# Performance work log

Hardware: AMD Instinct MI355X
Metric: run time of the kernel (lower is better)

Reference implementation:

```python
import jax, jax.numpy as jnp
import numpy as np

N_NODES = 100000
N_EDGES = 1600000
HIDDEN = 128
OUT = 64
NUM_LAYERS = 3


def setup_inputs() -> dict:
    key = jax.random.key(0)
    k1, k2, k3 = jax.random.split(key, 3)
    x = jax.random.normal(k1, (N_NODES, HIDDEN), dtype=jnp.float32)
    edge_index = jax.random.randint(k2, (2, N_EDGES), 0, N_NODES, dtype=jnp.int64)
    W = jax.random.normal(k3, (OUT, HIDDEN), dtype=jnp.float32) * (1.0 / np.sqrt(HIDDEN))
    b = jnp.zeros((OUT,), dtype=jnp.float32)
    return {"x": x, "edge_index": edge_index, "W": W, "b": b}


def reference(x, edge_index, W, b):
    n = x.shape[0]
    row, col = edge_index[0], edge_index[1]
    # degree of destination nodes (bincount over row), clamped to >= 1
    deg = jax.ops.segment_sum(jnp.ones_like(row, dtype=x.dtype), row, num_segments=n)
    deg_inv_sqrt = jnp.clip(deg, 1.0, None) ** -0.5
    norm = (deg_inv_sqrt[row] * deg_inv_sqrt[col])[:, None]  # [E, 1]

    def propagate(h):
        # gather -> scale -> scatter-add
        return jax.ops.segment_sum(h[col] * norm, row, num_segments=n)

    embs = [x]
    h = x
    for _ in range(NUM_LAYERS):
        h = propagate(h)
        embs.append(h)
    out = jnp.mean(jnp.stack(embs, axis=0), axis=0)  # [N, HIDDEN]
    return out @ W.T + b
```

## Files before the change

kernel.cpp:

```cpp
#include <hip/hip_runtime.h>

#define N_NODES 100000
#define N_EDGES 1600000
#define HIDDEN  128
#define OUTF    64
#define SLOT    48

#define EDGE4BLKS ((N_EDGES / 4 + 255) / 256)
#define NODEBLKS  ((N_NODES + 255) / 256)

__device__ __forceinline__ unsigned short f2bf(float f) {
    unsigned u = __float_as_uint(f);
    u += 0x7fffu + ((u >> 16) & 1u);
    return (unsigned short)(u >> 16);
}
__device__ __forceinline__ float2 bfp2f(unsigned p) {
    return make_float2(__uint_as_float(p << 16), __uint_as_float(p & 0xffff0000u));
}

__global__ void prep_kernel(const float* __restrict__ W, float* __restrict__ Wt,
                            int4* __restrict__ cnt4,
                            int4* __restrict__ z0d, int4* __restrict__ z1d,
                            int4* __restrict__ z2d) {
    int bid = blockIdx.x, tid = threadIdx.x;
    if (bid < 98) {
        int i = bid * 256 + tid;
        if (i < N_NODES / 4) cnt4[i] = make_int4(0, 0, 0, 0);
    } else if (bid < 130) {
        int i = (bid - 98) * 256 + tid;
        if (i < HIDDEN * OUTF) {
            int o = i / HIDDEN, k = i % HIDDEN;
            Wt[k * OUTF + o] = W[i];
        }
    } else {
        if (tid < 8)       z0d[tid]      = make_int4(0, 0, 0, 0);
        else if (tid < 16) z1d[tid - 8]  = make_int4(0, 0, 0, 0);
        else if (tid < 24) z2d[tid - 16] = make_int4(0, 0, 0, 0);
    }
}

#define GR    64
#define BK    32
#define HSP   36
#define WTP   68
__global__ __launch_bounds__(256) void mega_a_kernel(const float* __restrict__ x,
                                                     const float* __restrict__ Wt,
                                                     unsigned short* __restrict__ y0,
                                                     const int* __restrict__ ei,
                                                     int* __restrict__ cnt,
                                                     int* __restrict__ rank) {
    __shared__ float hs[GR * HSP];
    __shared__ float wt[BK * WTP];
    int tid = threadIdx.x;

    if (blockIdx.x & 1) {
        int cb = blockIdx.x >> 1;
        int t  = cb * 256 + tid;
        int e0 = t * 4;
        if (e0 + 3 < N_EDGES) {
            int4 r4 = *(const int4*)(ei + e0);
            int k0 = atomicAdd(&cnt[r4.x], 1);
            int k1 = atomicAdd(&cnt[r4.y], 1);
            int k2 = atomicAdd(&cnt[r4.z], 1);
            int k3 = atomicAdd(&cnt[r4.w], 1);
            *(int4*)(rank + e0) = make_int4(k0, k1, k2, k3);
        } else {
            for (int e = e0; e < N_EDGES; ++e) rank[e] = atomicAdd(&cnt[ei[e]], 1);
        }
        return;
    }

    int rowBase = (blockIdx.x >> 1) * GR;
    int o4 = (tid & 15) * 4;
    int rq = (tid >> 4) * 4;
    float4 a0 = {0,0,0,0}, a1 = {0,0,0,0}, a2 = {0,0,0,0}, a3 = {0,0,0,0};

    for (int kt = 0; kt < HIDDEN / BK; ++kt) {
        if (kt) __syncthreads();
        int kbase = kt * BK;
        #pragma unroll
        for (int t = 0; t < 2; ++t) {
            int f = tid + t * 256;
            int r = f >> 3, c4 = (f & 7) * 4;
            int row = rowBase + r;
            float4 v = (row < N_NODES) ? *(const float4*)(x + (size_t)row * HIDDEN + kbase + c4)
                                       : make_float4(0.f, 0.f, 0.f, 0.f);
            *(float4*)&hs[r * HSP + c4] = v;
        }
        #pragma unroll
        for (int t = 0; t < 2; ++t) {
            int f = tid + t * 256;
            int k = f >> 4, c4 = (f & 15) * 4;
            float4 v = *(const float4*)(Wt + (size_t)(kbase + k) * OUTF + c4);
            *(float4*)&wt[k * WTP + c4] = v;
        }
        __syncthreads();
        #pragma unroll 8
        for (int kk = 0; kk < BK; ++kk) {
            float4 wv = *(const float4*)&wt[kk * WTP + o4];
            float h0 = hs[(rq + 0) * HSP + kk];
            float h1 = hs[(rq + 1) * HSP + kk];
            float h2 = hs[(rq + 2) * HSP + kk];
            float h3 = hs[(rq + 3) * HSP + kk];
            a0.x += h0 * wv.x; a0.y += h0 * wv.y; a0.z += h0 * wv.z; a0.w += h0 * wv.w;
            a1.x += h1 * wv.x; a1.y += h1 * wv.y; a1.z += h1 * wv.z; a1.w += h1 * wv.w;
            a2.x += h2 * wv.x; a2.y += h2 * wv.y; a2.z += h2 * wv.z; a2.w += h2 * wv.w;
            a3.x += h3 * wv.x; a3.y += h3 * wv.y; a3.z += h3 * wv.z; a3.w += h3 * wv.w;
        }
    }
    int row = rowBase + rq;
    #pragma unroll
    for (int r = 0; r < 4; ++r) {
        if (row + r < N_NODES) {
            float4 a = (r == 0) ? a0 : (r == 1) ? a1 : (r == 2) ? a2 : a3;
            ushort4 s = {f2bf(a.x), f2bf(a.y), f2bf(a.z), f2bf(a.w)};
            *(ushort4*)&y0[(size_t)(row + r) * OUTF + o4] = s;
        }
    }
}

__global__ void mega_b_kernel(const int* __restrict__ ei,
                              const int* __restrict__ rank,
                              int* __restrict__ csr,
                              const int* __restrict__ cnt,
                              float* __restrict__ dinv,
                              float* __restrict__ rdinv) {
    int bid = blockIdx.x, tid = threadIdx.x;
    if (bid < EDGE4BLKS) {
        int t  = bid * 256 + tid;
        int e0 = t * 4;
        if (e0 + 3 < N_EDGES) {
            int4 r4 = *(const int4*)(ei + e0);
            int4 c4 = *(const int4*)(ei + N_EDGES + e0);
            int4 k4 = *(const int4*)(rank + e0);
            if (k4.x < SLOT) csr[r4.x * SLOT + k4.x] = c4.x;
            if (k4.y < SLOT) csr[r4.y * SLOT + k4.y] = c4.y;
            if (k4.z < SLOT) csr[r4.z * SLOT + k4.z] = c4.z;
            if (k4.w < SLOT) csr[r4.w * SLOT + k4.w] = c4.w;
        } else {
            for (int e = e0; e < N_EDGES; ++e) {
                int k = rank[e];
                if (k < SLOT) csr[ei[e] * SLOT + k] = ei[N_EDGES + e];
            }
        }
    } else {
        int i = (bid - EDGE4BLKS) * 256 + tid;
        if (i < N_NODES) {
            int deg  = cnt[i];
            float d  = fmaxf((float)deg, 1.0f);
            dinv[i]  = rsqrtf(d);
            rdinv[i] = sqrtf(d);
            if (i == 0) dinv[N_NODES] = 0.0f;
            int dc = deg > SLOT ? SLOT : deg;
            int dp = (dc + 7) & ~7;
            #pragma unroll
            for (int j = 0; j < 7; ++j)
                if (dc + j < dp) csr[i * SLOT + dc + j] = N_NODES;
        }
    }
}

__global__ __launch_bounds__(256) void pull1_kernel(const int* __restrict__ cnt,
                                                    const int* __restrict__ csr,
                                                    const float* __restrict__ dinv,
                                                    const unsigned short* __restrict__ y0,
                                                    unsigned short* __restrict__ z1) {
    int node = blockIdx.x * 4 + (threadIdx.x >> 6);
    int lane = threadIdx.x & 63;
    if (node >= N_NODES) return;
    int half = lane >> 5;
    int fp   = (lane & 31) * 2;
    int deg  = cnt[node];
    if (deg > SLOT) deg = SLOT;
    int degp = (deg + 7) & ~7;
    int s = node * SLOT;
    int e = s + degp;
    float2 acc = make_float2(0.f, 0.f);
    int i = s;
    for (; i + 15 < e; i += 16) {
        int c0 = csr[i      + half];
        int c1 = csr[i +  2 + half];
        int c2 = csr[i +  4 + half];
        int c3 = csr[i +  6 + half];
        int c4 = csr[i +  8 + half];
        int c5 = csr[i + 10 + half];
        int c6 = csr[i + 12 + half];
        int c7 = csr[i + 14 + half];
        float d0 = dinv[c0], d1 = dinv[c1], d2 = dinv[c2], d3 = dinv[c3];
        float d4 = dinv[c4], d5 = dinv[c5], d6 = dinv[c6], d7 = dinv[c7];
        unsigned p0 = *(const unsigned*)(y0 + (size_t)c0 * OUTF + fp);
        unsigned p1 = *(const unsigned*)(y0 + (size_t)c1 * OUTF + fp);
        unsigned p2 = *(const unsigned*)(y0 + (size_t)c2 * OUTF + fp);
        unsigned p3 = *(const unsigned*)(y0 + (size_t)c3 * OUTF + fp);
        unsigned p4 = *(const unsigned*)(y0 + (size_t)c4 * OUTF + fp);
        unsigned p5 = *(const unsigned*)(y0 + (size_t)c5 * OUTF + fp);
        unsigned p6 = *(const unsigned*)(y0 + (size_t)c6 * OUTF + fp);
        unsigned p7 = *(const unsigned*)(y0 + (size_t)c7 * OUTF + fp);
        float2 v0 = bfp2f(p0), v1 = bfp2f(p1), v2 = bfp2f(p2), v3 = bfp2f(p3);
        float2 v4 = bfp2f(p4), v5 = bfp2f(p5), v6 = bfp2f(p6), v7 = bfp2f(p7);
        acc.x += d0*v0.x + d1*v1.x + d2*v2.x + d3*v3.x + d4*v4.x + d5*v5.x + d6*v6.x + d7*v7.x;
        acc.y += d0*v0.y + d1*v1.y + d2*v2.y + d3*v3.y + d4*v4.y + d5*v5.y + d6*v6.y + d7*v7.y;
    }
    if (i < e) {
        int c0 = csr[i     + half];
        int c1 = csr[i + 2 + half];
        int c2 = csr[i + 4 + half];
        int c3 = csr[i + 6 + half];
        float d0 = dinv[c0], d1 = dinv[c1], d2 = dinv[c2], d3 = dinv[c3];
        unsigned p0 = *(const unsigned*)(y0 + (size_t)c0 * OUTF + fp);
        unsigned p1 = *(const unsigned*)(y0 + (size_t)c1 * OUTF + fp);
        unsigned p2 = *(const unsigned*)(y0 + (size_t)c2 * OUTF + fp);
        unsigned p3 = *(const unsigned*)(y0 + (size_t)c3 * OUTF + fp);
        float2 v0 = bfp2f(p0), v1 = bfp2f(p1), v2 = bfp2f(p2), v3 = bfp2f(p3);
        acc.x += d0*v0.x + d1*v1.x + d2*v2.x + d3*v3.x;
        acc.y += d0*v0.y + d1*v1.y + d2*v2.y + d3*v3.y;
    }
    acc.x += __shfl_xor(acc.x, 32);
    acc.y += __shfl_xor(acc.y, 32);
    if (lane < 32) {
        float dn = dinv[node];
        float zs = dn * dn;
        ushort2 o = {f2bf(acc.x * zs), f2bf(acc.y * zs)};
        *(ushort2*)(z1 + (size_t)node * OUTF + fp) = o;
    }
}

__global__ __launch_bounds__(256) void pull_kernel(const int* __restrict__ cnt,
                                                   const int* __restrict__ csr,
                                                   const float* __restrict__ dinv,
                                                   const unsigned short* __restrict__ zsrc,
                                                   unsigned short* __restrict__ zdst) {
    int node = blockIdx.x * 4 + (threadIdx.x >> 6);
    int lane = threadIdx.x & 63;
    if (node >= N_NODES) return;
    int half = lane >> 5;
    int fp   = (lane & 31) * 2;
    int deg  = cnt[node];
    if (deg > SLOT) deg = SLOT;
    int degp = (deg + 7) & ~7;
    int s = node * SLOT;
    int e = s + degp;
    float2 acc = make_float2(0.f, 0.f);
    int i = s;
    for (; i + 15 < e; i += 16) {
        int c0 = csr[i      + half];
        int c1 = csr[i +  2 + half];
        int c2 = csr[i +  4 + half];
        int c3 = csr[i +  6 + half];
        int c4 = csr[i +  8 + half];
        int c5 = csr[i + 10 + half];
        int c6 = csr[i + 12 + half];
        int c7 = csr[i + 14 + half];
        unsigned p0 = *(const unsigned*)(zsrc + (size_t)c0 * OUTF + fp);
        unsigned p1 = *(const unsigned*)(zsrc + (size_t)c1 * OUTF + fp);
        unsigned p2 = *(const unsigned*)(zsrc + (size_t)c2 * OUTF + fp);
        unsigned p3 = *(const unsigned*)(zsrc + (size_t)c3 * OUTF + fp);
        unsigned p4 = *(const unsigned*)(zsrc + (size_t)c4 * OUTF + fp);
        unsigned p5 = *(const unsigned*)(zsrc + (size_t)c5 * OUTF + fp);
        unsigned p6 = *(const unsigned*)(zsrc + (size_t)c6 * OUTF + fp);
        unsigned p7 = *(const unsigned*)(zsrc + (size_t)c7 * OUTF + fp);
        float2 v0 = bfp2f(p0), v1 = bfp2f(p1), v2 = bfp2f(p2), v3 = bfp2f(p3);
        float2 v4 = bfp2f(p4), v5 = bfp2f(p5), v6 = bfp2f(p6), v7 = bfp2f(p7);
        acc.x += (v0.x + v1.x) + (v2.x + v3.x) + (v4.x + v5.x) + (v6.x + v7.x);
        acc.y += (v0.y + v1.y) + (v2.y + v3.y) + (v4.y + v5.y) + (v6.y + v7.y);
    }
    if (i < e) {
        int c0 = csr[i     + half];
        int c1 = csr[i + 2 + half];
        int c2 = csr[i + 4 + half];
        int c3 = csr[i + 6 + half];
        unsigned p0 = *(const unsigned*)(zsrc + (size_t)c0 * OUTF + fp);
        unsigned p1 = *(const unsigned*)(zsrc + (size_t)c1 * OUTF + fp);
        unsigned p2 = *(const unsigned*)(zsrc + (size_t)c2 * OUTF + fp);
        unsigned p3 = *(const unsigned*)(zsrc + (size_t)c3 * OUTF + fp);
        float2 v0 = bfp2f(p0), v1 = bfp2f(p1), v2 = bfp2f(p2), v3 = bfp2f(p3);
        acc.x += (v0.x + v1.x) + (v2.x + v3.x);
        acc.y += (v0.y + v1.y) + (v2.y + v3.y);
    }
    acc.x += __shfl_xor(acc.x, 32);
    acc.y += __shfl_xor(acc.y, 32);
    if (lane < 32) {
        float dn = dinv[node];
        float zs = dn * dn;
        ushort2 o = {f2bf(acc.x * zs), f2bf(acc.y * zs)};
        *(ushort2*)(zdst + (size_t)node * OUTF + fp) = o;
    }
}

__global__ __launch_bounds__(256) void pull_merge_kernel(const int* __restrict__ cnt,
                                                         const int* __restrict__ csr,
                                                         const float* __restrict__ dinv,
                                                         const float* __restrict__ rdinv,
                                                         const unsigned short* __restrict__ y0,
                                                         const unsigned short* __restrict__ z1,
                                                         const unsigned short* __restrict__ z2,
                                                         const float* __restrict__ b,
                                                         float* __restrict__ out) {
    int node = blockIdx.x * 4 + (threadIdx.x >> 6);
    int lane = threadIdx.x & 63;
    if (node >= N_NODES) return;
    int half = lane >> 5;
    int fp   = (lane & 31) * 2;
    int deg  = cnt[node];
    if (deg > SLOT) deg = SLOT;
    int degp = (deg + 7) & ~7;
    int s = node * SLOT;
    int e = s + degp;
    float2 acc = make_float2(0.f, 0.f);
    int i = s;
    for (; i + 15 < e; i += 16) {
        int c0 = csr[i      + half];
        int c1 = csr[i +  2 + half];
        int c2 = csr[i +  4 + half];
        int c3 = csr[i +  6 + half];
        int c4 = csr[i +  8 + half];
        int c5 = csr[i + 10 + half];
        int c6 = csr[i + 12 + half];
        int c7 = csr[i + 14 + half];
        unsigned p0 = *(const unsigned*)(z2 + (size_t)c0 * OUTF + fp);
        unsigned p1 = *(const unsigned*)(z2 + (size_t)c1 * OUTF + fp);
        unsigned p2 = *(const unsigned*)(z2 + (size_t)c2 * OUTF + fp);
        unsigned p3 = *(const unsigned*)(z2 + (size_t)c3 * OUTF + fp);
        unsigned p4 = *(const unsigned*)(z2 + (size_t)c4 * OUTF + fp);
        unsigned p5 = *(const unsigned*)(z2 + (size_t)c5 * OUTF + fp);
        unsigned p6 = *(const unsigned*)(z2 + (size_t)c6 * OUTF + fp);
        unsigned p7 = *(const unsigned*)(z2 + (size_t)c7 * OUTF + fp);
        float2 v0 = bfp2f(p0), v1 = bfp2f(p1), v2 = bfp2f(p2), v3 = bfp2f(p3);
        float2 v4 = bfp2f(p4), v5 = bfp2f(p5), v6 = bfp2f(p6), v7 = bfp2f(p7);
        acc.x += (v0.x + v1.x) + (v2.x + v3.x) + (v4.x + v5.x) + (v6.x + v7.x);
        acc.y += (v0.y + v1.y) + (v2.y + v3.y) + (v4.y + v5.y) + (v6.y + v7.y);
    }
    if (i < e) {
        int c0 = csr[i     + half];
        int c1 = csr[i + 2 + half];
        int c2 = csr[i + 4 + half];
        int c3 = csr[i + 6 + half];
        unsigned p0 = *(const unsigned*)(z2 + (size_t)c0 * OUTF + fp);
        unsigned p1 = *(const unsigned*)(z2 + (size_t)c1 * OUTF + fp);
        unsigned p2 = *(const unsigned*)(z2 + (size_t)c2 * OUTF + fp);
        unsigned p3 = *(const unsigned*)(z2 + (size_t)c3 * OUTF + fp);
        float2 v0 = bfp2f(p0), v1 = bfp2f(p1), v2 = bfp2f(p2), v3 = bfp2f(p3);
        acc.x += (v0.x + v1.x) + (v2.x + v3.x);
        acc.y += (v0.y + v1.y) + (v2.y + v3.y);
    }
    acc.x += __shfl_xor(acc.x, 32);
    acc.y += __shfl_xor(acc.y, 32);
    if (lane < 32) {
        size_t idx = (size_t)node * OUTF + fp;
        float rd = rdinv[node];
        float dn = dinv[node];
        float2 s0 = bfp2f(*(const unsigned*)(y0 + idx));
        float2 s1 = bfp2f(*(const unsigned*)(z1 + idx));
        float2 s2 = bfp2f(*(const unsigned*)(z2 + idx));
        float2 bv = *(const float2*)(b + fp);
        float2 r;
        r.x = 0.25f * ((dn * s0.x + s1.x + s2.x) * rd + dn * acc.x) + bv.x;
        r.y = 0.25f * ((dn * s0.y + s1.y + s2.y) * rd + dn * acc.y) + bv.y;
        *(float2*)(out + idx) = r;
    }
}

extern "C" void kernel_launch(void* const* d_in, const int* in_sizes, int n_in,
                              void* d_out, int out_size, void* d_ws, size_t ws_size,
                              hipStream_t stream) {
    const float* x  = (const float*)d_in[0];
    const int*   ei = (const int*)d_in[1];
    const float* W  = (const float*)d_in[2];
    const float* b  = (const float*)d_in[3];
    float*       out = (float*)d_out;

    const size_t ZROWS = (size_t)N_NODES + 1;
    unsigned short* y0 = (unsigned short*)d_ws;
    unsigned short* z1 = y0 + ZROWS * OUTF;
    unsigned short* z2 = z1 + ZROWS * OUTF;
    float* Wt      = (float*)(z2 + ZROWS * OUTF);
    int*   csr     = (int*)(Wt + HIDDEN * OUTF);
    int*   cnt     = csr + (size_t)N_NODES * SLOT;
    float* dinv    = (float*)(cnt + N_NODES);
    float* rdinv   = dinv + (N_NODES + 1);

    int* rank = (int*)z2;

    const int BLK = 256;
    const int pullBlocks = (N_NODES + 3) / 4;

    prep_kernel<<<131, BLK, 0, stream>>>(W, Wt, (int4*)cnt,
                                         (int4*)(y0 + (size_t)N_NODES * OUTF),
                                         (int4*)(z1 + (size_t)N_NODES * OUTF),
                                         (int4*)(z2 + (size_t)N_NODES * OUTF));
    mega_a_kernel<<<2 * EDGE4BLKS, BLK, 0, stream>>>(x, Wt, y0, ei, cnt, rank);
    mega_b_kernel<<<EDGE4BLKS + NODEBLKS, BLK, 0, stream>>>(ei, rank, csr, cnt, dinv, rdinv);
    pull1_kernel<<<pullBlocks, BLK, 0, stream>>>(cnt, csr, dinv, y0, z1);
    pull_kernel<<<pullBlocks, BLK, 0, stream>>>(cnt, csr, dinv, z1, z2);
    pull_merge_kernel<<<pullBlocks, BLK, 0, stream>>>(cnt, csr, dinv, rdinv,
                                                      y0, z1, z2, b, out);
}
```

Before: 297.1 us.

## Pack four nodes per wavefront with 16-byte vectorized bf16 row gathers

The pull kernels are rewritten so each 64-lane wavefront handles four nodes instead of one. Each node gets 16 lanes: 8 lanes of 16-byte feature chunks times 2 edge parities. Gathers of bf16 rows become uint4 loads with eight float accumulators per lane, and the first two pull kernels are merged into one template. This cuts the number of load instructions and raises memory-level parallelism for low-degree nodes. The cost is higher register pressure, and lanes within a wavefront may diverge when their nodes have different degrees.

```diff
diff --git a/kernel.cpp b/kernel.cpp
--- a/kernel.cpp
+++ b/kernel.cpp
@@ -8,6 +8,7 @@
 
 #define EDGE4BLKS ((N_EDGES / 4 + 255) / 256)
 #define NODEBLKS  ((N_NODES + 255) / 256)
+#define PULLBLKS  ((N_NODES + 15) / 16)
 
 __device__ __forceinline__ unsigned short f2bf(float f) {
     unsigned u = __float_as_uint(f);
@@ -16,6 +17,9 @@
 }
 __device__ __forceinline__ float2 bfp2f(unsigned p) {
     return make_float2(__uint_as_float(p << 16), __uint_as_float(p & 0xffff0000u));
+}
+__device__ __forceinline__ unsigned packbf(float a, float b) {
+    return (unsigned)f2bf(a) | ((unsigned)f2bf(b) << 16);
 }
 
 __global__ void prep_kernel(const float* __restrict__ W, float* __restrict__ Wt,
@@ -160,203 +164,172 @@
     }
 }
 
-__global__ __launch_bounds__(256) void pull1_kernel(const int* __restrict__ cnt,
-                                                    const int* __restrict__ csr,
-                                                    const float* __restrict__ dinv,
-                                                    const unsigned short* __restrict__ y0,
-                                                    unsigned short* __restrict__ z1) {
-    int node = blockIdx.x * 4 + (threadIdx.x >> 6);
+template<bool SC>
+__global__ __launch_bounds__(256) void pull_v2_kernel(const int* __restrict__ cnt,
+                                                      const int* __restrict__ csr,
+                                                      const float* __restrict__ dinv,
+                                                      const unsigned short* __restrict__ zsrc,
+                                                      unsigned short* __restrict__ zdst) {
     int lane = threadIdx.x & 63;
-    if (node >= N_NODES) return;
-    int half = lane >> 5;
-    int fp   = (lane & 31) * 2;
-    int deg  = cnt[node];
+    int wid  = (blockIdx.x * blockDim.x + threadIdx.x) >> 6;
+    int g    = lane >> 3;
+    int node = wid * 4 + (g >> 1);
+    int par  = g & 1;
+    int fo   = (lane & 7) * 8;
+    bool valid = node < N_NODES;
+    int deg = valid ? cnt[node] : 0;
     if (deg > SLOT) deg = SLOT;
     int degp = (deg + 7) & ~7;
     int s = node * SLOT;
-    int e = s + degp;
-    float2 acc = make_float2(0.f, 0.f);
-    int i = s;
-    for (; i + 15 < e; i += 16) {
-        int c0 = csr[i      + half];
-        int c1 = csr[i +  2 + half];
-        int c2 = csr[i +  4 + half];
-        int c3 = csr[i +  6 + half];
-        int c4 = csr[i +  8 + half];
-        int c5 = csr[i + 10 + half];
-        int c6 = csr[i + 12 + half];
-        int c7 = csr[i + 14 + half];
-        float d0 = dinv[c0], d1 = dinv[c1], d2 = dinv[c2], d3 = dinv[c3];
-        float d4 = dinv[c4], d5 = dinv[c5], d6 = dinv[c6], d7 = dinv[c7];
-        unsigned p0 = *(const unsigned*)(y0 + (size_t)c0 * OUTF + fp);
-        unsigned p1 = *(const unsigned*)(y0 + (size_t)c1 * OUTF + fp);
-        unsigned p2 = *(const unsigned*)(y0 + (size_t)c2 * OUTF + fp);
-        unsigned p3 = *(const unsigned*)(y0 + (size_t)c3 * OUTF + fp);
-        unsigned p4 = *(const unsigned*)(y0 + (size_t)c4 * OUTF + fp);
-        unsigned p5 = *(const unsigned*)(y0 + (size_t)c5 * OUTF + fp);
-        unsigned p6 = *(const unsigned*)(y0 + (size_t)c6 * OUTF + fp);
-        unsigned p7 = *(const unsigned*)(y0 + (size_t)c7 * OUTF + fp);
-        float2 v0 = bfp2f(p0), v1 = bfp2f(p1), v2 = bfp2f(p2), v3 = bfp2f(p3);
-        float2 v4 = bfp2f(p4), v5 = bfp2f(p5), v6 = bfp2f(p6), v7 = bfp2f(p7);
-        acc.x += d0*v0.x + d1*v1.x + d2*v2.x + d3*v3.x + d4*v4.x + d5*v5.x + d6*v6.x + d7*v7.x;
-        acc.y += d0*v0.y + d1*v1.y + d2*v2.y + d3*v3.y + d4*v4.y + d5*v5.y + d6*v6.y + d7*v7.y;
-    }
-    if (i < e) {
-        int c0 = csr[i     + half];
-        int c1 = csr[i + 2 + half];
-        int c2 = csr[i + 4 + half];
-        int c3 = csr[i + 6 + half];
-        float d0 = dinv[c0], d1 = dinv[c1], d2 = dinv[c2], d3 = dinv[c3];
-        unsigned p0 = *(const unsigned*)(y0 + (size_t)c0 * OUTF + fp);
-        unsigned p1 = *(const unsigned*)(y0 + (size_t)c1 * OUTF + fp);
-        unsigned p2 = *(const unsigned*)(y0 + (size_t)c2 * OUTF + fp);
-        unsigned p3 = *(const unsigned*)(y0 + (size_t)c3 * OUTF + fp);
-        float2 v0 = bfp2f(p0), v1 = bfp2f(p1), v2 = bfp2f(p2), v3 = bfp2f(p3);
-        acc.x += d0*v0.x + d1*v1.x + d2*v2.x + d3*v3.x;
-        acc.y += d0*v0.y + d1*v1.y + d2*v2.y + d3*v3.y;
-    }
-    acc.x += __shfl_xor(acc.x, 32);
-    acc.y += __shfl_xor(acc.y, 32);
-    if (lane < 32) {
+    float a0=0.f,a1=0.f,a2=0.f,a3=0.f,a4=0.f,a5=0.f,a6=0.f,a7=0.f;
+
+    int e16 = degp & ~15;
+    int i = 0;
+    for (; i < e16; i += 16) {
+        int c0 = csr[s + i +  0 + par];
+        int c1 = csr[s + i +  2 + par];
+        int c2 = csr[s + i +  4 + par];
+        int c3 = csr[s + i +  6 + par];
+        int c4 = csr[s + i +  8 + par];
+        int c5 = csr[s + i + 10 + par];
+        int c6 = csr[s + i + 12 + par];
+        int c7 = csr[s + i + 14 + par];
+        float d0=1.f,d1=1.f,d2=1.f,d3=1.f,d4=1.f,d5=1.f,d6=1.f,d7=1.f;
+        if (SC) {
+            d0 = dinv[c0]; d1 = dinv[c1]; d2 = dinv[c2]; d3 = dinv[c3];
+            d4 = dinv[c4]; d5 = dinv[c5]; d6 = dinv[c6]; d7 = dinv[c7];
+        }
+        uint4 p0 = *(const uint4*)(zsrc + (size_t)c0 * OUTF + fo);
+        uint4 p1 = *(const uint4*)(zsrc + (size_t)c1 * OUTF + fo);
+        uint4 p2 = *(const uint4*)(zsrc + (size_t)c2 * OUTF + fo);
+        uint4 p3 = *(const uint4*)(zsrc + (size_t)c3 * OUTF + fo);
+        uint4 p4 = *(const uint4*)(zsrc + (size_t)c4 * OUTF + fo);
+        uint4 p5 = *(const uint4*)(zsrc + (size_t)c5 * OUTF + fo);
+        uint4 p6 = *(const uint4*)(zsrc + (size_t)c6 * OUTF + fo);
+        uint4 p7 = *(const uint4*)(zsrc + (size_t)c7 * OUTF + fo);
+        #define ACC(P, D) { \
+            float2 q0 = bfp2f(P.x), q1 = bfp2f(P.y), q2 = bfp2f(P.z), q3 = bfp2f(P.w); \
+            a0 += D*q0.x; a1 += D*q0.y; a2 += D*q1.x; a3 += D*q1.y; \
+            a4 += D*q2.x; a5 += D*q2.y; a6 += D*q3.x; a7 += D*q3.y; }
+        ACC(p0, d0) ACC(p1, d1) ACC(p2, d2) ACC(p3, d3)
+        ACC(p4, d4) ACC(p5, d5) ACC(p6, d6) ACC(p7, d7)
+    }
+    if (degp & 8) {
+        int c0 = csr[s + i + 0 + par];
+        int c1 = csr[s + i + 2 + par];
+        int c2 = csr[s + i + 4 + par];
+        int c3 = csr[s + i + 6 + par];
+        float d0=1.f,d1=1.f,d2=1.f,d3=1.f;
+        if (SC) { d0 = dinv[c0]; d1 = dinv[c1]; d2 = dinv[c2]; d3 = dinv[c3]; }
+        uint4 p0 = *(const uint4*)(zsrc + (size_t)c0 * OUTF + fo);
+        uint4 p1 = *(const uint4*)(zsrc + (size_t)c1 * OUTF + fo);
+        uint4 p2 = *(const uint4*)(zsrc + (size_t)c2 * OUTF + fo);
+        uint4 p3 = *(const uint4*)(zsrc + (size_t)c3 * OUTF + fo);
+        ACC(p0, d0) ACC(p1, d1) ACC(p2, d2) ACC(p3, d3)
+        #undef ACC
+    }
+    a0 += __shfl_xor(a0, 8); a1 += __shfl_xor(a1, 8);
+    a2 += __shfl_xor(a2, 8); a3 += __shfl_xor(a3, 8);
+    a4 += __shfl_xor(a4, 8); a5 += __shfl_xor(a5, 8);
+    a6 += __shfl_xor(a6, 8); a7 += __shfl_xor(a7, 8);
+    if ((lane & 8) == 0 && valid) {
         float dn = dinv[node];
         float zs = dn * dn;
-        ushort2 o = {f2bf(acc.x * zs), f2bf(acc.y * zs)};
-        *(ushort2*)(z1 + (size_t)node * OUTF + fp) = o;
-    }
-}
-
-__global__ __launch_bounds__(256) void pull_kernel(const int* __restrict__ cnt,
-                                                   const int* __restrict__ csr,
-                                                   const float* __restrict__ dinv,
-                                                   const unsigned short* __restrict__ zsrc,
-                                                   unsigned short* __restrict__ zdst) {
-    int node = blockIdx.x * 4 + (threadIdx.x >> 6);
+        uint4 o;
+        o.x = packbf(a0 * zs, a1 * zs);
+        o.y = packbf(a2 * zs, a3 * zs);
+        o.z = packbf(a4 * zs, a5 * zs);
+        o.w = packbf(a6 * zs, a7 * zs);
+        *(uint4*)(zdst + (size_t)node * OUTF + fo) = o;
+    }
+}
+
+__global__ __launch_bounds__(256) void pull_merge_v2_kernel(const int* __restrict__ cnt,
+                                                            const int* __restrict__ csr,
+                                                            const float* __restrict__ dinv,
+                                                            const float* __restrict__ rdinv,
+                                                            const unsigned short* __restrict__ y0,
+                                                            const unsigned short* __restrict__ z1,
+                                                            const unsigned short* __restrict__ z2,
+                                                            const float* __restrict__ b,
+                                                            float* __restrict__ out) {
     int lane = threadIdx.x & 63;
-    if (node >= N_NODES) return;
-    int half = lane >> 5;
-    int fp   = (lane & 31) * 2;
-    int deg  = cnt[node];
+    int wid  = (blockIdx.x * blockDim.x + threadIdx.x) >> 6;
+    int g    = lane >> 3;
+    int node = wid * 4 + (g >> 1);
+    int par  = g & 1;
+    int fo   = (lane & 7) * 8;
+    bool valid = node < N_NODES;
+    int deg = valid ? cnt[node] : 0;
     if (deg > SLOT) deg = SLOT;
     int degp = (deg + 7) & ~7;
     int s = node * SLOT;
-    int e = s + degp;
-    float2 acc = make_float2(0.f, 0.f);
-    int i = s;
-    for (; i + 15 < e; i += 16) {
-        int c0 = csr[i      + half];
-        int c1 = csr[i +  2 + half];
-        int c2 = csr[i +  4 + half];
-        int c3 = csr[i +  6 + half];
-        int c4 = csr[i +  8 + half];
-        int c5 = csr[i + 10 + half];
-        int c6 = csr[i + 12 + half];
-        int c7 = csr[i + 14 + half];
-        unsigned p0 = *(const unsigned*)(zsrc + (size_t)c0 * OUTF + fp);
-        unsigned p1 = *(const unsigned*)(zsrc + (size_t)c1 * OUTF + fp);
-        unsigned p2 = *(const unsigned*)(zsrc + (size_t)c2 * OUTF + fp);
-        unsigned p3 = *(const unsigned*)(zsrc + (size_t)c3 * OUTF + fp);
-        unsigned p4 = *(const unsigned*)(zsrc + (size_t)c4 * OUTF + fp);
-        unsigned p5 = *(const unsigned*)(zsrc + (size_t)c5 * OUTF + fp);
-        unsigned p6 = *(const unsigned*)(zsrc + (size_t)c6 * OUTF + fp);
-        unsigned p7 = *(const unsigned*)(zsrc + (size_t)c7 * OUTF + fp);
-        float2 v0 = bfp2f(p0), v1 = bfp2f(p1), v2 = bfp2f(p2), v3 = bfp2f(p3);
-        float2 v4 = bfp2f(p4), v5 = bfp2f(p5), v6 = bfp2f(p6), v7 = bfp2f(p7);
-        acc.x += (v0.x + v1.x) + (v2.x + v3.x) + (v4.x + v5.x) + (v6.x + v7.x);
-        acc.y += (v0.y + v1.y) + (v2.y + v3.y) + (v4.y + v5.y) + (v6.y + v7.y);
-    }
-    if (i < e) {
-        int c0 = csr[i     + half];
-        int c1 = csr[i + 2 + half];
-        int c2 = csr[i + 4 + half];
-        int c3 = csr[i + 6 + half];
-        unsigned p0 = *(const unsigned*)(zsrc + (size_t)c0 * OUTF + fp);
-        unsigned p1 = *(const unsigned*)(zsrc + (size_t)c1 * OUTF + fp);
-        unsigned p2 = *(const unsigned*)(zsrc + (size_t)c2 * OUTF + fp);
-        unsigned p3 = *(const unsigned*)(zsrc + (size_t)c3 * OUTF + fp);
-        float2 v0 = bfp2f(p0), v1 = bfp2f(p1), v2 = bfp2f(p2), v3 = bfp2f(p3);
-        acc.x += (v0.x + v1.x) + (v2.x + v3.x);
-        acc.y += (v0.y + v1.y) + (v2.y + v3.y);
-    }
-    acc.x += __shfl_xor(acc.x, 32);
-    acc.y += __shfl_xor(acc.y, 32);
-    if (lane < 32) {
+    float a0=0.f,a1=0.f,a2=0.f,a3=0.f,a4=0.f,a5=0.f,a6=0.f,a7=0.f;
+
+    int e16 = degp & ~15;
+    int i = 0;
+    for (; i < e16; i += 16) {
+        int c0 = csr[s + i +  0 + par];
+        int c1 = csr[s + i +  2 + par];
+        int c2 = csr[s + i +  4 + par];
+        int c3 = csr[s + i +  6 + par];
+        int c4 = csr[s + i +  8 + par];
+        int c5 = csr[s + i + 10 + par];
+        int c6 = csr[s + i + 12 + par];
+        int c7 = csr[s + i + 14 + par];
+        uint4 p0 = *(const uint4*)(z2 + (size_t)c0 * OUTF + fo);
+        uint4 p1 = *(const uint4*)(z2 + (size_t)c1 * OUTF + fo);
+        uint4 p2 = *(const uint4*)(z2 + (size_t)c2 * OUTF + fo);
+        uint4 p3 = *(const uint4*)(z2 + (size_t)c3 * OUTF + fo);
+        uint4 p4 = *(const uint4*)(z2 + (size_t)c4 * OUTF + fo);
+        uint4 p5 = *(const uint4*)(z2 + (size_t)c5 * OUTF + fo);
+        uint4 p6 = *(const uint4*)(z2 + (size_t)c6 * OUTF + fo);
+        uint4 p7 = *(const uint4*)(z2 + (size_t)c7 * OUTF + fo);
+        #define ACC1(P) { \
+            float2 q0 = bfp2f(P.x), q1 = bfp2f(P.y), q2 = bfp2f(P.z), q3 = bfp2f(P.w); \
+            a0 += q0.x; a1 += q0.y; a2 += q1.x; a3 += q1.y; \
+            a4 += q2.x; a5 += q2.y; a6 += q3.x; a7 += q3.y; }
+        ACC1(p0) ACC1(p1) ACC1(p2) ACC1(p3) ACC1(p4) ACC1(p5) ACC1(p6) ACC1(p7)
+    }
+    if (degp & 8) {
+        int c0 = csr[s + i + 0 + par];
+        int c1 = csr[s + i + 2 + par];
+        int c2 = csr[s + i + 4 + par];
+        int c3 = csr[s + i + 6 + par];
+        uint4 p0 = *(const uint4*)(z2 + (size_t)c0 * OUTF + fo);
+        uint4 p1 = *(const uint4*)(z2 + (size_t)c1 * OUTF + fo);
+        uint4 p2 = *(const uint4*)(z2 + (size_t)c2 * OUTF + fo);
+        uint4 p3 = *(const uint4*)(z2 + (size_t)c3 * OUTF + fo);
+        ACC1(p0) ACC1(p1) ACC1(p2) ACC1(p3)
+        #undef ACC1
+    }
+    a0 += __shfl_xor(a0, 8); a1 += __shfl_xor(a1, 8);
+    a2 += __shfl_xor(a2, 8); a3 += __shfl_xor(a3, 8);
+    a4 += __shfl_xor(a4, 8); a5 += __shfl_xor(a5, 8);
+    a6 += __shfl_xor(a6, 8); a7 += __shfl_xor(a7, 8);
+    if ((lane & 8) == 0 && valid) {
+        size_t idx = (size_t)node * OUTF + fo;
         float dn = dinv[node];
-        float zs = dn * dn;
-        ushort2 o = {f2bf(acc.x * zs), f2bf(acc.y * zs)};
-        *(ushort2*)(zdst + (size_t)node * OUTF + fp) = o;
-    }
-}
-
-__global__ __launch_bounds__(256) void pull_merge_kernel(const int* __restrict__ cnt,
-                                                         const int* __restrict__ csr,
-                                                         const float* __restrict__ dinv,
-                                                         const float* __restrict__ rdinv,
-                                                         const unsigned short* __restrict__ y0,
-                                                         const unsigned short* __restrict__ z1,
-                                                         const unsigned short* __restrict__ z2,
-                                                         const float* __restrict__ b,
-                                                         float* __restrict__ out) {
-    int node = blockIdx.x * 4 + (threadIdx.x >> 6);
-    int lane = threadIdx.x & 63;
-    if (node >= N_NODES) return;
-    int half = lane >> 5;
-    int fp   = (lane & 31) * 2;
-    int deg  = cnt[node];
-    if (deg > SLOT) deg = SLOT;
-    int degp = (deg + 7) & ~7;
-    int s = node * SLOT;
-    int e = s + degp;
-    float2 acc = make_float2(0.f, 0.f);
-    int i = s;
-    for (; i + 15 < e; i += 16) {
-        int c0 = csr[i      + half];
-        int c1 = csr[i +  2 + half];
-        int c2 = csr[i +  4 + half];
-        int c3 = csr[i +  6 + half];
-        int c4 = csr[i +  8 + half];
-        int c5 = csr[i + 10 + half];
-        int c6 = csr[i + 12 + half];
-        int c7 = csr[i + 14 + half];
-        unsigned p0 = *(const unsigned*)(z2 + (size_t)c0 * OUTF + fp);
-        unsigned p1 = *(const unsigned*)(z2 + (size_t)c1 * OUTF + fp);
-        unsigned p2 = *(const unsigned*)(z2 + (size_t)c2 * OUTF + fp);
-        unsigned p3 = *(const unsigned*)(z2 + (size_t)c3 * OUTF + fp);
-        unsigned p4 = *(const unsigned*)(z2 + (size_t)c4 * OUTF + fp);
-        unsigned p5 = *(const unsigned*)(z2 + (size_t)c5 * OUTF + fp);
-        unsigned p6 = *(const unsigned*)(z2 + (size_t)c6 * OUTF + fp);
-        unsigned p7 = *(const unsigned*)(z2 + (size_t)c7 * OUTF + fp);
-        float2 v0 = bfp2f(p0), v1 = bfp2f(p1), v2 = bfp2f(p2), v3 = bfp2f(p3);
-        float2 v4 = bfp2f(p4), v5 = bfp2f(p5), v6 = bfp2f(p6), v7 = bfp2f(p7);
-        acc.x += (v0.x + v1.x) + (v2.x + v3.x) + (v4.x + v5.x) + (v6.x + v7.x);
-        acc.y += (v0.y + v1.y) + (v2.y + v3.y) + (v4.y + v5.y) + (v6.y + v7.y);
-    }
-    if (i < e) {
-        int c0 = csr[i     + half];
-        int c1 = csr[i + 2 + half];
-        int c2 = csr[i + 4 + half];
-        int c3 = csr[i + 6 + half];
-        unsigned p0 = *(const unsigned*)(z2 + (size_t)c0 * OUTF + fp);
-        unsigned p1 = *(const unsigned*)(z2 + (size_t)c1 * OUTF + fp);
-        unsigned p2 = *(const unsigned*)(z2 + (size_t)c2 * OUTF + fp);
-        unsigned p3 = *(const unsigned*)(z2 + (size_t)c3 * OUTF + fp);
-        float2 v0 = bfp2f(p0), v1 = bfp2f(p1), v2 = bfp2f(p2), v3 = bfp2f(p3);
-        acc.x += (v0.x + v1.x) + (v2.x + v3.x);
-        acc.y += (v0.y + v1.y) + (v2.y + v3.y);
-    }
-    acc.x += __shfl_xor(acc.x, 32);
-    acc.y += __shfl_xor(acc.y, 32);
-    if (lane < 32) {
-        size_t idx = (size_t)node * OUTF + fp;
         float rd = rdinv[node];
-        float dn = dinv[node];
-        float2 s0 = bfp2f(*(const unsigned*)(y0 + idx));
-        float2 s1 = bfp2f(*(const unsigned*)(z1 + idx));
-        float2 s2 = bfp2f(*(const unsigned*)(z2 + idx));
-        float2 bv = *(const float2*)(b + fp);
-        float2 r;
-        r.x = 0.25f * ((dn * s0.x + s1.x + s2.x) * rd + dn * acc.x) + bv.x;
-        r.y = 0.25f * ((dn * s0.y + s1.y + s2.y) * rd + dn * acc.y) + bv.y;
-        *(float2*)(out + idx) = r;
+        uint4 py = *(const uint4*)(y0 + idx);
+        uint4 pz1 = *(const uint4*)(z1 + idx);
+        uint4 pz2 = *(const uint4*)(z2 + idx);
+        float4 bv0 = *(const float4*)(b + fo);
+        float4 bv1 = *(const float4*)(b + fo + 4);
+        float2 y_0 = bfp2f(py.x), y_1 = bfp2f(py.y), y_2 = bfp2f(py.z), y_3 = bfp2f(py.w);
+        float2 u_0 = bfp2f(pz1.x), u_1 = bfp2f(pz1.y), u_2 = bfp2f(pz1.z), u_3 = bfp2f(pz1.w);
+        float2 v_0 = bfp2f(pz2.x), v_1 = bfp2f(pz2.y), v_2 = bfp2f(pz2.z), v_3 = bfp2f(pz2.w);
+        float4 r0, r1;
+        r0.x = 0.25f * ((dn * y_0.x + u_0.x + v_0.x) * rd + dn * a0) + bv0.x;
+        r0.y = 0.25f * ((dn * y_0.y + u_0.y + v_0.y) * rd + dn * a1) + bv0.y;
+        r0.z = 0.25f * ((dn * y_1.x + u_1.x + v_1.x) * rd + dn * a2) + bv0.z;
+        r0.w = 0.25f * ((dn * y_1.y + u_1.y + v_1.y) * rd + dn * a3) + bv0.w;
+        r1.x = 0.25f * ((dn * y_2.x + u_2.x + v_2.x) * rd + dn * a4) + bv1.x;
+        r1.y = 0.25f * ((dn * y_2.y + u_2.y + v_2.y) * rd + dn * a5) + bv1.y;
+        r1.z = 0.25f * ((dn * y_3.x + u_3.x + v_3.x) * rd + dn * a6) + bv1.z;
+        r1.w = 0.25f * ((dn * y_3.y + u_3.y + v_3.y) * rd + dn * a7) + bv1.w;
+        *(float4*)(out + idx) = r0;
+        *(float4*)(out + idx + 4) = r1;
     }
 }
 
@@ -382,7 +355,6 @@
     int* rank = (int*)z2;
 
     const int BLK = 256;
-    const int pullBlocks = (N_NODES + 3) / 4;
 
     prep_kernel<<<131, BLK, 0, stream>>>(W, Wt, (int4*)cnt,
                                          (int4*)(y0 + (size_t)N_NODES * OUTF),
@@ -390,8 +362,8 @@
                                          (int4*)(z2 + (size_t)N_NODES * OUTF));
     mega_a_kernel<<<2 * EDGE4BLKS, BLK, 0, stream>>>(x, Wt, y0, ei, cnt, rank);
     mega_b_kernel<<<EDGE4BLKS + NODEBLKS, BLK, 0, stream>>>(ei, rank, csr, cnt, dinv, rdinv);
-    pull1_kernel<<<pullBlocks, BLK, 0, stream>>>(cnt, csr, dinv, y0, z1);
-    pull_kernel<<<pullBlocks, BLK, 0, stream>>>(cnt, csr, dinv, z1, z2);
-    pull_merge_kernel<<<pullBlocks, BLK, 0, stream>>>(cnt, csr, dinv, rdinv,
-                                                      y0, z1, z2, b, out);
-}
+    pull_v2_kernel<true><<<PULLBLKS, BLK, 0, stream>>>(cnt, csr, dinv, y0, z1);
+    pull_v2_kernel<false><<<PULLBLKS, BLK, 0, stream>>>(cnt, csr, dinv, z1, z2);
+    pull_merge_v2_kernel<<<PULLBLKS, BLK, 0, stream>>>(cnt, csr, dinv, rdinv,
+                                                       y0, z1, z2, b, out);
+}
```

After: 282.3 us. 1.05x faster.
